# Kernel optimization log

Measured on AMD Instinct MI355X. Metric: run time of the kernel, lower is better.

The kernel has to match this reference:

```python
import jax, jax.numpy as jnp
import numpy as np

B, S, H, NH, PF, L, V = 8, 1024, 1024, 16, 4096, 6, 32000
HD = H // NH
STD = 0.02
NEG = -1e10


def setup_inputs() -> dict:
    key = jax.random.key(0)
    ks = jax.random.split(key, 12)
    inp = {
        "src": jax.random.randint(ks[0], (B, S), 0, V),
        "src_mask": jnp.ones((B, 1, 1, S), dtype=bool),
        "tok_emb": jax.random.normal(ks[1], (V, H), jnp.float32) * STD,
        "pos_emb": jax.random.normal(ks[2], (S, H), jnp.float32) * STD,
        "Wq": jax.random.normal(ks[3], (L, H, H), jnp.float32) * STD,
        "bq": jnp.zeros((L, H), jnp.float32),
        "Wk": jax.random.normal(ks[4], (L, H, H), jnp.float32) * STD,
        "bk": jnp.zeros((L, H), jnp.float32),
        "Wv": jax.random.normal(ks[5], (L, H, H), jnp.float32) * STD,
        "bv": jnp.zeros((L, H), jnp.float32),
        "Wo": jax.random.normal(ks[6], (L, H, H), jnp.float32) * STD,
        "bo": jnp.zeros((L, H), jnp.float32),
        "W1": jax.random.normal(ks[7], (L, H, PF), jnp.float32) * STD,
        "b1": jnp.zeros((L, PF), jnp.float32),
        "W2": jax.random.normal(ks[8], (L, PF, H), jnp.float32) * STD,
        "b2": jnp.zeros((L, H), jnp.float32),
        "ln1_g": jnp.ones((L, H), jnp.float32),
        "ln1_b": jnp.zeros((L, H), jnp.float32),
        "ln2_g": jnp.ones((L, H), jnp.float32),
        "ln2_b": jnp.zeros((L, H), jnp.float32),
    }
    return inp


def layer_norm(x, g, b, eps=1e-5):
    m = jnp.mean(x, axis=-1, keepdims=True)
    v = jnp.mean((x - m) ** 2, axis=-1, keepdims=True)
    return (x - m) * jax.lax.rsqrt(v + eps) * g + b


def reference(src, src_mask, tok_emb, pos_emb, Wq, bq, Wk, bk, Wv, bv, Wo, bo,
              W1, b1, W2, b2, ln1_g, ln1_b, ln2_g, ln2_b):
    # embedding * sqrt(hid_dim) + positional embedding (dropout = identity at eval)
    x = tok_emb[src] * jnp.sqrt(jnp.float32(H)) + pos_emb[None, :S]
    attn_scale = jnp.sqrt(jnp.float32(HD))
    for l in range(L):
        # multi-head self-attention
        q = (x @ Wq[l] + bq[l]).reshape(B, S, NH, HD).transpose(0, 2, 1, 3)
        k = (x @ Wk[l] + bk[l]).reshape(B, S, NH, HD).transpose(0, 2, 1, 3)
        v = (x @ Wv[l] + bv[l]).reshape(B, S, NH, HD).transpose(0, 2, 1, 3)
        energy = jnp.einsum('bhqd,bhkd->bhqk', q, k) / attn_scale  # [B,NH,S,S]
        energy = jnp.where(src_mask, energy, NEG)
        attn = jax.nn.softmax(energy, axis=-1)
        o = jnp.einsum('bhqk,bhkd->bhqd', attn, v)
        o = o.transpose(0, 2, 1, 3).reshape(B, S, H) @ Wo[l] + bo[l]
        x = layer_norm(x + o, ln1_g[l], ln1_b[l])
        # position-wise feedforward
        f = jax.nn.relu(x @ W1[l] + b1[l]) @ W2[l] + b2[l]
        x = layer_norm(x + f, ln2_g[l], ln2_b[l])
    return x
```

## Files before the change

### kernel.cpp

```cpp
#include <hip/hip_runtime.h>
#include <cstdint>
#include <cstddef>


#define DI __device__ __forceinline__

typedef __attribute__((ext_vector_type(8))) short short8;
typedef __attribute__((ext_vector_type(4))) short s16x4;
typedef __attribute__((ext_vector_type(4))) float f32x4;
typedef __attribute__((ext_vector_type(4))) unsigned u32x4;

static constexpr int H  = 1024;
static constexpr int S  = 1024;
static constexpr int BB = 8;
static constexpr int NH = 16;
static constexpr int PF = 4096;
static constexpr int M  = BB * S;
static constexpr int L  = 6;

DI short f2bf(float f) {
  unsigned u = __builtin_bit_cast(unsigned, f);
  u += 0x7fffu + ((u >> 16) & 1u);
  return (short)(u >> 16);
}

DI unsigned packbf(float a, float b) {
  return (__builtin_bit_cast(unsigned, a) >> 16) |
         (__builtin_bit_cast(unsigned, b) & 0xffff0000u);
}

DI void async16(void* lds, const void* g) {
  __builtin_amdgcn_global_load_lds(
      (const __attribute__((address_space(1))) unsigned*)g,
      (__attribute__((address_space(3))) unsigned*)lds, 16, 0, 0);
}

DI f32x4 mfma16(short8 a, short8 b, f32x4 c) {
  return __builtin_amdgcn_mfma_f32_16x16x32_bf16(a, b, c, 0, 0, 0);
}

__global__ __launch_bounds__(256) void embed_kernel(
    const int* __restrict__ src, const float* __restrict__ tok,
    const float* __restrict__ pos, float* __restrict__ xf,
    short* __restrict__ xb) {
  const int row = blockIdx.x;
  const int s = row & (S - 1);
  const int i0 = threadIdx.x << 2;
  const int v = src[row];
  const float4 te = *(const float4*)(tok + (size_t)v * H + i0);
  const float4 pe = *(const float4*)(pos + (size_t)s * H + i0);
  float o[4] = {te.x * 32.f + pe.x, te.y * 32.f + pe.y,
                te.z * 32.f + pe.z, te.w * 32.f + pe.w};
  *(float4*)(xf + (size_t)row * H + i0) = make_float4(o[0], o[1], o[2], o[3]);
  s16x4 pk;
  pk[0] = f2bf(o[0]); pk[1] = f2bf(o[1]); pk[2] = f2bf(o[2]); pk[3] = f2bf(o[3]);
  *(s16x4*)(xb + (size_t)row * H + i0) = pk;
}

__global__ __launch_bounds__(256) void wconv_kernel(
    const float* __restrict__ W, short* __restrict__ Wt, int K, int N) {
  __shared__ float tile[64][65];
  const int ntn = N >> 6;
  const int k0 = (blockIdx.x / ntn) << 6;
  const int n0 = (blockIdx.x % ntn) << 6;
  const int r4 = threadIdx.x >> 6, cc = threadIdx.x & 63;
#pragma unroll
  for (int i = 0; i < 16; i++) {
    const int r = (i << 2) + r4;
    tile[r][cc] = W[(size_t)(k0 + r) * N + n0 + cc];
  }
  __syncthreads();
#pragma unroll
  for (int i = 0; i < 16; i++) {
    const int n = (i << 2) + r4;
    Wt[(size_t)(n0 + n) * K + k0 + cc] = f2bf(tile[cc][n]);
  }
}

template <int EPI>
__global__ __launch_bounds__(256, 4) void gemm128(
    const short* __restrict__ A, const short* __restrict__ Bt,
    const float* __restrict__ bias, void* __restrict__ out,
    const int N, const int K) {
  __shared__ char lds[32768];
  const int tid = threadIdx.x;
  const int w = tid >> 6, lane = tid & 63;
  const int g = lane >> 4, ci = lane & 15;
  const int wm = w >> 1, wn = w & 1;
  const int nbn = N >> 7;
  const int bid = (int)blockIdx.x;
  const int swz = (bid & 7) * ((int)gridDim.x >> 3) + (bid >> 3);
  const int brow = (swz / nbn) << 7;
  const int bcol = (swz % nbn) << 7;

  const int srow = lane >> 2;
  const int schk = ((lane & 3) ^ ((lane >> 3) & 3)) << 3;
  const short* aS0 = A + (size_t)(brow + w * 16 + srow) * K + schk;
  const short* aS1 = A + (size_t)(brow + w * 16 + 64 + srow) * K + schk;
  const short* bS0 = Bt + (size_t)(bcol + w * 16 + srow) * K + schk;
  const short* bS1 = Bt + (size_t)(bcol + w * 16 + 64 + srow) * K + schk;

  int aoff[4], boff[4];
  const int swzc = (g ^ ((ci >> 1) & 3)) << 4;
#pragma unroll
  for (int i = 0; i < 4; i++) {
    aoff[i] = (wm * 64 + i * 16 + ci) * 64 + swzc;
    boff[i] = 8192 + (wn * 64 + i * 16 + ci) * 64 + swzc;
  }

  auto stage = [&](int kh, int buf) {
    char* base = lds + buf * 16384;
    const int ko = kh << 5;
    async16(base + w * 1024, aS0 + ko);
    async16(base + 4096 + w * 1024, aS1 + ko);
    async16(base + 8192 + w * 1024, bS0 + ko);
    async16(base + 12288 + w * 1024, bS1 + ko);
  };

  f32x4 acc[4][4];
#pragma unroll
  for (int a = 0; a < 4; a++)
#pragma unroll
    for (int c = 0; c < 4; c++) acc[a][c] = f32x4{0.f, 0.f, 0.f, 0.f};

  stage(0, 0);
  stage(1, 1);
  asm volatile("s_waitcnt vmcnt(4)" ::: "memory");
  __builtin_amdgcn_sched_barrier(0);
  __builtin_amdgcn_s_barrier();

  const int nt = K >> 5;
  for (int t = 0; t < nt; t++) {
    const char* cb = lds + (t & 1) * 16384;
    short8 afr[4], bfr[4];
#pragma unroll
    for (int mi = 0; mi < 4; mi++) afr[mi] = *(const short8*)(cb + aoff[mi]);
#pragma unroll
    for (int nj = 0; nj < 4; nj++) bfr[nj] = *(const short8*)(cb + boff[nj]);
    asm volatile("s_waitcnt lgkmcnt(0)" ::: "memory");
    __builtin_amdgcn_sched_barrier(0);
    __builtin_amdgcn_s_barrier();
    if (t + 2 < nt) stage(t + 2, t & 1);
    __builtin_amdgcn_s_setprio(1);
#pragma unroll
    for (int mi = 0; mi < 4; mi++)
#pragma unroll
      for (int nj = 0; nj < 4; nj++)
        acc[mi][nj] = mfma16(afr[mi], bfr[nj], acc[mi][nj]);
    __builtin_amdgcn_s_setprio(0);
    if (t + 2 < nt) asm volatile("s_waitcnt vmcnt(4)" ::: "memory");
    else            asm volatile("s_waitcnt vmcnt(0)" ::: "memory");
    __builtin_amdgcn_sched_barrier(0);
    if (t + 1 < nt) __builtin_amdgcn_s_barrier();
  }

  if constexpr (EPI <= 2) {
#pragma unroll
    for (int mi = 0; mi < 4; mi++) {
      float bv[4];
#pragma unroll
      for (int nj = 0; nj < 4; nj++)
        bv[nj] = bias[bcol + wn * 64 + nj * 16 + ci];
#pragma unroll
      for (int r = 0; r < 4; r++) {
        const int row = brow + wm * 64 + mi * 16 + (g << 2) + r;
#pragma unroll
        for (int nj = 0; nj < 4; nj++) {
          const int col = bcol + wn * 64 + nj * 16 + ci;
          float vv = acc[mi][nj][r] + bv[nj];
          if constexpr (EPI == 1) vv = fmaxf(vv, 0.f);
          if constexpr (EPI == 2) ((float*)out)[(size_t)row * N + col] = vv;
          else ((short*)out)[(size_t)row * N + col] = f2bf(vv);
        }
      }
    }
  } else {
    __syncthreads();
    short* bb = (short*)lds;
    const int bI = brow >> 10, s0 = brow & (S - 1);
    short* o = (short*)out;
#pragma unroll
    for (int hh = 0; hh < 2; hh++) {
      if (wn == hh) {
#pragma unroll
        for (int nj = 0; nj < 4; nj++) {
          const int d = nj * 16 + ci;
          const float bv = bias[bcol + hh * 64 + d];
#pragma unroll
          for (int mi = 0; mi < 4; mi++) {
            const int sl = wm * 64 + mi * 16 + (g << 2);
            s16x4 pk;
#pragma unroll
            for (int r = 0; r < 4; r++) pk[r] = f2bf(acc[mi][nj][r] + bv);
            *(s16x4*)(bb + d * 136 + sl) = pk;
          }
        }
      }
      __syncthreads();
#pragma unroll
      for (int jj = 0; jj < 4; jj++) {
        const int d = tid >> 2, sc = (tid & 3) + jj * 4;
        const short8 v = *(const short8*)(bb + d * 136 + sc * 8);
        *(short8*)(o + ((size_t)bI * H + bcol + hh * 64 + d) * S + s0 + sc * 8) = v;
      }
      __syncthreads();
    }
  }
}

__global__ __launch_bounds__(256) void attn_kernel(
    const short* __restrict__ q, const short* __restrict__ k,
    const short* __restrict__ vt, short* __restrict__ ao) {
  __shared__ short lsk[2][4096];
  __shared__ short lsv[2][4096];
  const int tid = threadIdx.x;
  const int w = tid >> 6, lane = tid & 63;
  const int g = lane >> 4, ci = lane & 15;
  const int bid = ((int)blockIdx.x & 7) * 256 + ((int)blockIdx.x >> 3);
  const int qt = bid & 15;
  const int bh = bid >> 4;
  const int b = bh >> 4, h = bh & 15;
  const int hbase = h << 6;

  const int r8 = lane >> 3, c8 = lane & 7;
  const int cs = c8 ^ r8;
  const short* kbase = k + ((size_t)b * S) * H + hbase;
  const short* vbase = vt + ((size_t)b * H + hbase) * S;

  const size_t qrow = (size_t)b * S + (qt << 6) + (w << 4) + ci;
  short8 qf[2];
#pragma unroll
  for (int ks = 0; ks < 2; ks++)
    qf[ks] = *(const short8*)(q + qrow * H + hbase + ks * 32 + (g << 3));

  const int swz = ci & 7;
  int koff[2], voff[2][2];
#pragma unroll
  for (int ks = 0; ks < 2; ks++) {
    koff[ks] = ci * 128 + (((4 * ks + g) ^ swz) << 4);
#pragma unroll
    for (int pc = 0; pc < 2; pc++)
      voff[ks][pc] =
          ci * 128 + (((4 * ks + 2 * pc + (g >> 1)) ^ swz) << 4) + ((g & 1) << 3);
  }

#pragma unroll
  for (int t = 0; t < 2; t++) {
    const int row = (w << 3) + t * 32 + r8;
    async16(&lsk[0][t * 2048 + (w << 9)], kbase + (size_t)row * H + cs * 8);
    async16(&lsv[0][t * 2048 + (w << 9)], vbase + (size_t)row * S + cs * 8);
  }
  __syncthreads();

  const f32x4 zero = {0.f, 0.f, 0.f, 0.f};
  f32x4 of[4];
#pragma unroll
  for (int nf = 0; nf < 4; nf++) of[nf] = zero;
  float mrun = -INFINITY, lsum = 0.f;

#pragma unroll 2
  for (int kt = 0; kt < 16; kt++) {
    const int cur = kt & 1;
    if (kt < 15) {
      const int kr1 = (kt + 1) << 6;
#pragma unroll
      for (int t = 0; t < 2; t++) {
        const int row = (w << 3) + t * 32 + r8;
        async16(&lsk[cur ^ 1][t * 2048 + (w << 9)],
                kbase + (size_t)(kr1 + row) * H + cs * 8);
        async16(&lsv[cur ^ 1][t * 2048 + (w << 9)],
                vbase + (size_t)row * S + kr1 + cs * 8);
      }
    }
    const char* kb = (const char*)lsk[cur];
    const char* vb = (const char*)lsv[cur];

    f32x4 st[4];
#pragma unroll
    for (int mf = 0; mf < 4; mf++) st[mf] = zero;
#pragma unroll
    for (int ks = 0; ks < 2; ks++)
#pragma unroll
      for (int mf = 0; mf < 4; mf++) {
        const short8 kf = *(const short8*)(kb + koff[ks] + mf * 2048);
        st[mf] = mfma16(kf, qf[ks], st[mf]);
      }

    float tmax = -INFINITY;
#pragma unroll
    for (int mf = 0; mf < 4; mf++)
#pragma unroll
      for (int r = 0; r < 4; r++) tmax = fmaxf(tmax, st[mf][r]);
    tmax = fmaxf(tmax, __shfl_xor(tmax, 16));
    tmax = fmaxf(tmax, __shfl_xor(tmax, 32));
    const float mnew = fmaxf(mrun, tmax * 0.125f);
    const float alpha = __expf(mrun - mnew);
    float rs = 0.f;
    float p[4][4];
#pragma unroll
    for (int mf = 0; mf < 4; mf++)
#pragma unroll
      for (int r = 0; r < 4; r++) {
        p[mf][r] = __expf(__builtin_fmaf(st[mf][r], 0.125f, -mnew));
        rs += p[mf][r];
      }
    rs += __shfl_xor(rs, 16);
    rs += __shfl_xor(rs, 32);
    lsum = lsum * alpha + rs;
    mrun = mnew;

    unsigned pk[4][2];
#pragma unroll
    for (int mf = 0; mf < 4; mf++) {
      pk[mf][0] = packbf(p[mf][0], p[mf][1]);
      pk[mf][1] = packbf(p[mf][2], p[mf][3]);
    }
#pragma unroll
    for (int nf = 0; nf < 4; nf++)
#pragma unroll
      for (int r = 0; r < 4; r++) of[nf][r] *= alpha;

#pragma unroll
    for (int ks = 0; ks < 2; ks++) {
      u32x4 uu;
      uu[0] = pk[2 * ks][0];
      uu[1] = pk[2 * ks][1];
      uu[2] = pk[2 * ks + 1][0];
      uu[3] = pk[2 * ks + 1][1];
      const short8 pfrag = __builtin_bit_cast(short8, uu);
#pragma unroll
      for (int nf = 0; nf < 4; nf++) {
        union { short8 v8; s16x4 h[2]; } vv;
        vv.h[0] = *(const s16x4*)(vb + voff[ks][0] + nf * 2048);
        vv.h[1] = *(const s16x4*)(vb + voff[ks][1] + nf * 2048);
        of[nf] = mfma16(vv.v8, pfrag, of[nf]);
      }
    }
    __syncthreads();
  }

  const float inv = 1.f / lsum;
#pragma unroll
  for (int nf = 0; nf < 4; nf++) {
    s16x4 o4;
#pragma unroll
    for (int r = 0; r < 4; r++) o4[r] = f2bf(of[nf][r] * inv);
    *(s16x4*)(ao + qrow * H + hbase + (nf << 4) + (g << 2)) = o4;
  }
}

__global__ __launch_bounds__(256) void ln_kernel(
    const float* __restrict__ x, const float* __restrict__ t,
    const float* __restrict__ gm, const float* __restrict__ bt,
    float* __restrict__ yf, short* __restrict__ yb) {
  const int row = blockIdx.x;
  const int i0 = threadIdx.x << 2;
  const size_t base = (size_t)row * H + i0;
  const float4 a = *(const float4*)(x + base);
  const float4 bb = *(const float4*)(t + base);
  float v[4] = {a.x + bb.x, a.y + bb.y, a.z + bb.z, a.w + bb.w};
  float s = v[0] + v[1] + v[2] + v[3];
  float qq = v[0] * v[0] + v[1] * v[1] + v[2] * v[2] + v[3] * v[3];
#pragma unroll
  for (int off = 32; off; off >>= 1) {
    s += __shfl_down(s, off);
    qq += __shfl_down(qq, off);
  }
  __shared__ float red[8];
  const int w = threadIdx.x >> 6, lane = threadIdx.x & 63;
  if (lane == 0) { red[w] = s; red[4 + w] = qq; }
  __syncthreads();
  s = red[0] + red[1] + red[2] + red[3];
  qq = red[4] + red[5] + red[6] + red[7];
  const float mean = s * (1.f / H);
  float var = qq * (1.f / H) - mean * mean;
  var = fmaxf(var, 0.f);
  const float rstd = rsqrtf(var + 1e-5f);
  const float4 gv = *(const float4*)(gm + i0);
  const float4 bv = *(const float4*)(bt + i0);
  float y[4] = {(v[0] - mean) * rstd * gv.x + bv.x,
                (v[1] - mean) * rstd * gv.y + bv.y,
                (v[2] - mean) * rstd * gv.z + bv.z,
                (v[3] - mean) * rstd * gv.w + bv.w};
  *(float4*)(yf + base) = make_float4(y[0], y[1], y[2], y[3]);
  s16x4 pk;
  pk[0] = f2bf(y[0]); pk[1] = f2bf(y[1]); pk[2] = f2bf(y[2]); pk[3] = f2bf(y[3]);
  *(s16x4*)(yb + base) = pk;
}

extern "C" void kernel_launch(void* const* d_in, const int* in_sizes, int n_in,
                              void* d_out, int out_size, void* d_ws, size_t ws_size,
                              hipStream_t stream) {
  const int* src = (const int*)d_in[0];
  const float* tok = (const float*)d_in[2];
  const float* pos = (const float*)d_in[3];
  const float* Wq = (const float*)d_in[4];
  const float* bq = (const float*)d_in[5];
  const float* Wk = (const float*)d_in[6];
  const float* bk = (const float*)d_in[7];
  const float* Wv = (const float*)d_in[8];
  const float* bv = (const float*)d_in[9];
  const float* Wo = (const float*)d_in[10];
  const float* bo = (const float*)d_in[11];
  const float* W1 = (const float*)d_in[12];
  const float* b1 = (const float*)d_in[13];
  const float* W2 = (const float*)d_in[14];
  const float* b2 = (const float*)d_in[15];
  const float* g1 = (const float*)d_in[16];
  const float* be1 = (const float*)d_in[17];
  const float* g2 = (const float*)d_in[18];
  const float* be2 = (const float*)d_in[19];

  char* p = (char*)d_ws;
  auto take = [&](size_t bytes) {
    char* r = p;
    p += (bytes + 255) & ~(size_t)255;
    return r;
  };
  float* xf   = (float*)take((size_t)M * H * 4);
  short* xb   = (short*)take((size_t)M * H * 2);
  float* tmp  = (float*)take((size_t)M * H * 4);
  short* qb   = (short*)take((size_t)M * H * 2);
  short* kbuf = (short*)take((size_t)M * H * 2);
  short* vtb  = (short*)take((size_t)M * H * 2);
  short* aob  = (short*)take((size_t)M * H * 2);
  short* fb   = (short*)take((size_t)M * PF * 2);
  short* wtq  = (short*)take((size_t)H * H * 2);
  short* wtk  = (short*)take((size_t)H * H * 2);
  short* wtv  = (short*)take((size_t)H * H * 2);
  short* wto  = (short*)take((size_t)H * H * 2);
  short* wt1  = (short*)take((size_t)H * PF * 2);
  short* wt2  = (short*)take((size_t)H * PF * 2);

  embed_kernel<<<M, 256, 0, stream>>>(src, tok, pos, xf, xb);

  for (int l = 0; l < L; l++) {
    wconv_kernel<<<(H / 64) * (H / 64), 256, 0, stream>>>(Wq + (size_t)l * H * H, wtq, H, H);
    wconv_kernel<<<(H / 64) * (H / 64), 256, 0, stream>>>(Wk + (size_t)l * H * H, wtk, H, H);
    wconv_kernel<<<(H / 64) * (H / 64), 256, 0, stream>>>(Wv + (size_t)l * H * H, wtv, H, H);
    wconv_kernel<<<(H / 64) * (H / 64), 256, 0, stream>>>(Wo + (size_t)l * H * H, wto, H, H);
    wconv_kernel<<<(H / 64) * (PF / 64), 256, 0, stream>>>(W1 + (size_t)l * H * PF, wt1, H, PF);
    wconv_kernel<<<(PF / 64) * (H / 64), 256, 0, stream>>>(W2 + (size_t)l * PF * H, wt2, PF, H);

    gemm128<0><<<512, 256, 0, stream>>>(xb, wtq, bq + (size_t)l * H, qb, H, H);
    gemm128<0><<<512, 256, 0, stream>>>(xb, wtk, bk + (size_t)l * H, kbuf, H, H);
    gemm128<3><<<512, 256, 0, stream>>>(xb, wtv, bv + (size_t)l * H, vtb, H, H);
    attn_kernel<<<BB * NH * (S / 64), 256, 0, stream>>>(qb, kbuf, vtb, aob);
    gemm128<2><<<512, 256, 0, stream>>>(aob, wto, bo + (size_t)l * H, tmp, H, H);
    ln_kernel<<<M, 256, 0, stream>>>(xf, tmp, g1 + (size_t)l * H, be1 + (size_t)l * H, xf, xb);
    gemm128<1><<<2048, 256, 0, stream>>>(xb, wt1, b1 + (size_t)l * PF, fb, PF, H);
    gemm128<2><<<512, 256, 0, stream>>>(fb, wt2, b2 + (size_t)l * H, tmp, H, PF);
    float* yf = (l == L - 1) ? (float*)d_out : xf;
    ln_kernel<<<M, 256, 0, stream>>>(xf, tmp, g2 + (size_t)l * H, be2 + (size_t)l * H, yf, xb);
  }
}
```

Baseline: 2.392 ms.

## Use 256x128 triple-buffered GEMM tiles, fuse QKV GEMM and weight conversions

```diff
diff --git a/kernel.cpp b/kernel.cpp
--- a/kernel.cpp
+++ b/kernel.cpp
@@ -57,12 +57,31 @@
   *(s16x4*)(xb + (size_t)row * H + i0) = pk;
 }
 
-__global__ __launch_bounds__(256) void wconv_kernel(
-    const float* __restrict__ W, short* __restrict__ Wt, int K, int N) {
+__global__ __launch_bounds__(256) void wconv_layer(
+    const float* __restrict__ Wq, const float* __restrict__ Wk,
+    const float* __restrict__ Wv, const float* __restrict__ Wo,
+    const float* __restrict__ W1, const float* __restrict__ W2,
+    const float* __restrict__ bq, const float* __restrict__ bk,
+    const float* __restrict__ bv, short* __restrict__ tq,
+    short* __restrict__ tk, short* __restrict__ tv, short* __restrict__ to,
+    short* __restrict__ t1, short* __restrict__ t2, float* __restrict__ bqkv) {
+  const int id = blockIdx.x;
+  if (id >= 3072) {
+    const int i = (id - 3072) * 256 + threadIdx.x;
+    bqkv[i] = (i < 1024) ? bq[i] : (i < 2048) ? bk[i - 1024] : bv[i - 2048];
+    return;
+  }
+  const float* W; short* Wt; int K, N, lb;
+  if (id < 256)       { W = Wq; Wt = tq; K = 1024; N = 1024; lb = id; }
+  else if (id < 512)  { W = Wk; Wt = tk; K = 1024; N = 1024; lb = id - 256; }
+  else if (id < 768)  { W = Wv; Wt = tv; K = 1024; N = 1024; lb = id - 512; }
+  else if (id < 1024) { W = Wo; Wt = to; K = 1024; N = 1024; lb = id - 768; }
+  else if (id < 2048) { W = W1; Wt = t1; K = 1024; N = 4096; lb = id - 1024; }
+  else                { W = W2; Wt = t2; K = 4096; N = 1024; lb = id - 2048; }
   __shared__ float tile[64][65];
   const int ntn = N >> 6;
-  const int k0 = (blockIdx.x / ntn) << 6;
-  const int n0 = (blockIdx.x % ntn) << 6;
+  const int k0 = (lb / ntn) << 6;
+  const int n0 = (lb % ntn) << 6;
   const int r4 = threadIdx.x >> 6, cc = threadIdx.x & 63;
 #pragma unroll
   for (int i = 0; i < 16; i++) {
@@ -78,69 +97,79 @@
 }
 
 template <int EPI>
-__global__ __launch_bounds__(256, 4) void gemm128(
+__global__ __launch_bounds__(512, 2) void gemmT(
     const short* __restrict__ A, const short* __restrict__ Bt,
-    const float* __restrict__ bias, void* __restrict__ out,
-    const int N, const int K) {
-  __shared__ char lds[32768];
+    const float* __restrict__ bias, void* __restrict__ out0,
+    short* __restrict__ outK, short* __restrict__ outV,
+    const int nbn, const int outN, const int K) {
+  extern __shared__ char lds[];
+  constexpr int BUF = 49152;
   const int tid = threadIdx.x;
   const int w = tid >> 6, lane = tid & 63;
   const int g = lane >> 4, ci = lane & 15;
   const int wm = w >> 1, wn = w & 1;
-  const int nbn = N >> 7;
+
   const int bid = (int)blockIdx.x;
-  const int swz = (bid & 7) * ((int)gridDim.x >> 3) + (bid >> 3);
-  const int brow = (swz / nbn) << 7;
-  const int bcol = (swz % nbn) << 7;
-
-  const int srow = lane >> 2;
-  const int schk = ((lane & 3) ^ ((lane >> 3) & 3)) << 3;
-  const short* aS0 = A + (size_t)(brow + w * 16 + srow) * K + schk;
-  const short* aS1 = A + (size_t)(brow + w * 16 + 64 + srow) * K + schk;
-  const short* bS0 = Bt + (size_t)(bcol + w * 16 + srow) * K + schk;
-  const short* bS1 = Bt + (size_t)(bcol + w * 16 + 64 + srow) * K + schk;
-
-  int aoff[4], boff[4];
-  const int swzc = (g ^ ((ci >> 1) & 3)) << 4;
-#pragma unroll
-  for (int i = 0; i < 4; i++) {
-    aoff[i] = (wm * 64 + i * 16 + ci) * 64 + swzc;
-    boff[i] = 8192 + (wn * 64 + i * 16 + ci) * 64 + swzc;
-  }
-
-  auto stage = [&](int kh, int buf) {
-    char* base = lds + buf * 16384;
-    const int ko = kh << 5;
-    async16(base + w * 1024, aS0 + ko);
-    async16(base + 4096 + w * 1024, aS1 + ko);
-    async16(base + 8192 + w * 1024, bS0 + ko);
-    async16(base + 12288 + w * 1024, bS1 + ko);
+  const int xcd = bid & 7, ii = bid >> 3;
+  const int bm = ((xcd & 3) << 3) | (ii & 7);
+  const int bn = (xcd >> 2) * (nbn >> 1) + (ii >> 3);
+  const int brow = bm << 8;
+  const int bcol = bn << 7;
+
+  const int srow = tid >> 3;
+  const int schk = ((tid & 7) ^ (srow & 7)) << 3;
+  const short* aS[4];
+#pragma unroll
+  for (int j = 0; j < 4; j++)
+    aS[j] = A + (size_t)(brow + srow + j * 64) * K + schk;
+  const short* bS[2];
+#pragma unroll
+  for (int j = 0; j < 2; j++)
+    bS[j] = Bt + (size_t)(bcol + srow + j * 64) * K + schk;
+
+  auto stA = [&](int t2, int j) {
+    async16(lds + (t2 % 3) * BUF + (tid + j * 512) * 16, aS[j] + (t2 << 6));
   };
+  auto stB = [&](int t2, int j) {
+    async16(lds + (t2 % 3) * BUF + 32768 + (tid + j * 512) * 16,
+            bS[j] + (t2 << 6));
+  };
+
+  int aoff[2], boff[2];
+#pragma unroll
+  for (int ks = 0; ks < 2; ks++) {
+    const int chk = ((ks * 4 + g) ^ (ci & 7)) << 4;
+    aoff[ks] = (wm * 64 + ci) * 128 + chk;
+    boff[ks] = 32768 + (wn * 64 + ci) * 128 + chk;
+  }
 
   f32x4 acc[4][4];
 #pragma unroll
   for (int a = 0; a < 4; a++)
 #pragma unroll
-    for (int c = 0; c < 4; c++) acc[a][c] = f32x4{0.f, 0.f, 0.f, 0.f};
-
-  stage(0, 0);
-  stage(1, 1);
-  asm volatile("s_waitcnt vmcnt(4)" ::: "memory");
+    for (int b = 0; b < 4; b++) acc[a][b] = f32x4{0.f, 0.f, 0.f, 0.f};
+
+  stA(0, 0); stA(0, 1); stB(0, 0); stA(0, 2); stA(0, 3); stB(0, 1);
+  stA(1, 0); stA(1, 1); stB(1, 0); stA(1, 2); stA(1, 3); stB(1, 1);
+  asm volatile("s_waitcnt vmcnt(6)" ::: "memory");
   __builtin_amdgcn_sched_barrier(0);
   __builtin_amdgcn_s_barrier();
 
-  const int nt = K >> 5;
+  const int nt = K >> 6;
   for (int t = 0; t < nt; t++) {
-    const char* cb = lds + (t & 1) * 16384;
+    const char* cb = lds + (t % 3) * BUF;
+    const bool pf = (t + 2 < nt);
     short8 afr[4], bfr[4];
 #pragma unroll
-    for (int mi = 0; mi < 4; mi++) afr[mi] = *(const short8*)(cb + aoff[mi]);
-#pragma unroll
-    for (int nj = 0; nj < 4; nj++) bfr[nj] = *(const short8*)(cb + boff[nj]);
+    for (int mi = 0; mi < 4; mi++)
+      afr[mi] = *(const short8*)(cb + aoff[0] + mi * 2048);
+#pragma unroll
+    for (int nj = 0; nj < 4; nj++)
+      bfr[nj] = *(const short8*)(cb + boff[0] + nj * 2048);
+    if (pf) { stA(t + 2, 0); stA(t + 2, 1); stB(t + 2, 0); }
+    __builtin_amdgcn_s_barrier();
     asm volatile("s_waitcnt lgkmcnt(0)" ::: "memory");
     __builtin_amdgcn_sched_barrier(0);
-    __builtin_amdgcn_s_barrier();
-    if (t + 2 < nt) stage(t + 2, t & 1);
     __builtin_amdgcn_s_setprio(1);
 #pragma unroll
     for (int mi = 0; mi < 4; mi++)
@@ -148,62 +177,86 @@
       for (int nj = 0; nj < 4; nj++)
         acc[mi][nj] = mfma16(afr[mi], bfr[nj], acc[mi][nj]);
     __builtin_amdgcn_s_setprio(0);
-    if (t + 2 < nt) asm volatile("s_waitcnt vmcnt(4)" ::: "memory");
-    else            asm volatile("s_waitcnt vmcnt(0)" ::: "memory");
+    __builtin_amdgcn_s_barrier();
+#pragma unroll
+    for (int mi = 0; mi < 4; mi++)
+      afr[mi] = *(const short8*)(cb + aoff[1] + mi * 2048);
+#pragma unroll
+    for (int nj = 0; nj < 4; nj++)
+      bfr[nj] = *(const short8*)(cb + boff[1] + nj * 2048);
+    if (pf) { stA(t + 2, 2); stA(t + 2, 3); stB(t + 2, 1); }
+    __builtin_amdgcn_s_barrier();
+    asm volatile("s_waitcnt lgkmcnt(0)" ::: "memory");
     __builtin_amdgcn_sched_barrier(0);
-    if (t + 1 < nt) __builtin_amdgcn_s_barrier();
-  }
-
-  if constexpr (EPI <= 2) {
+    __builtin_amdgcn_s_setprio(1);
+#pragma unroll
+    for (int mi = 0; mi < 4; mi++)
+#pragma unroll
+      for (int nj = 0; nj < 4; nj++)
+        acc[mi][nj] = mfma16(afr[mi], bfr[nj], acc[mi][nj]);
+    __builtin_amdgcn_s_setprio(0);
+    if (pf) asm volatile("s_waitcnt vmcnt(6)" ::: "memory");
+    else    asm volatile("s_waitcnt vmcnt(0)" ::: "memory");
+    __builtin_amdgcn_sched_barrier(0);
+    __builtin_amdgcn_s_barrier();
+  }
+
+  const bool vpath = (EPI == 4) && (bcol >= 2048);
+  if (!vpath) {
+    short* oq; const short* dummy; (void)dummy;
+    int bc = bcol;
+    if constexpr (EPI == 4) {
+      oq = (bcol >> 10) ? outK : (short*)out0;
+      bc = bcol & 1023;
+    }
+    float bv[4];
+#pragma unroll
+    for (int nj = 0; nj < 4; nj++)
+      bv[nj] = bias[bcol + wn * 64 + nj * 16 + ci];
 #pragma unroll
     for (int mi = 0; mi < 4; mi++) {
-      float bv[4];
-#pragma unroll
-      for (int nj = 0; nj < 4; nj++)
-        bv[nj] = bias[bcol + wn * 64 + nj * 16 + ci];
 #pragma unroll
       for (int r = 0; r < 4; r++) {
         const int row = brow + wm * 64 + mi * 16 + (g << 2) + r;
 #pragma unroll
         for (int nj = 0; nj < 4; nj++) {
-          const int col = bcol + wn * 64 + nj * 16 + ci;
+          const int col = bc + wn * 64 + nj * 16 + ci;
           float vv = acc[mi][nj][r] + bv[nj];
           if constexpr (EPI == 1) vv = fmaxf(vv, 0.f);
-          if constexpr (EPI == 2) ((float*)out)[(size_t)row * N + col] = vv;
-          else ((short*)out)[(size_t)row * N + col] = f2bf(vv);
-        }
-      }
-    }
-  } else {
-    __syncthreads();
-    short* bb = (short*)lds;
-    const int bI = brow >> 10, s0 = brow & (S - 1);
-    short* o = (short*)out;
-#pragma unroll
-    for (int hh = 0; hh < 2; hh++) {
-      if (wn == hh) {
-#pragma unroll
-        for (int nj = 0; nj < 4; nj++) {
-          const int d = nj * 16 + ci;
-          const float bv = bias[bcol + hh * 64 + d];
-#pragma unroll
-          for (int mi = 0; mi < 4; mi++) {
-            const int sl = wm * 64 + mi * 16 + (g << 2);
-            s16x4 pk;
-#pragma unroll
-            for (int r = 0; r < 4; r++) pk[r] = f2bf(acc[mi][nj][r] + bv);
-            *(s16x4*)(bb + d * 136 + sl) = pk;
+          if constexpr (EPI == 2) {
+            ((float*)out0)[(size_t)row * outN + col] = vv;
+          } else if constexpr (EPI == 4) {
+            oq[(size_t)row * outN + col] = f2bf(vv);
+          } else {
+            ((short*)out0)[(size_t)row * outN + col] = f2bf(vv);
           }
         }
       }
-      __syncthreads();
-#pragma unroll
-      for (int jj = 0; jj < 4; jj++) {
-        const int d = tid >> 2, sc = (tid & 3) + jj * 4;
-        const short8 v = *(const short8*)(bb + d * 136 + sc * 8);
-        *(short8*)(o + ((size_t)bI * H + bcol + hh * 64 + d) * S + s0 + sc * 8) = v;
+    }
+  } else {
+    __syncthreads();
+    short* tb = (short*)lds;
+#pragma unroll
+    for (int nj = 0; nj < 4; nj++) {
+      const int d = wn * 64 + nj * 16 + ci;
+      const float bv = bias[bcol + d];
+#pragma unroll
+      for (int mi = 0; mi < 4; mi++) {
+        const int s = wm * 64 + mi * 16 + (g << 2);
+        s16x4 pk;
+#pragma unroll
+        for (int r = 0; r < 4; r++) pk[r] = f2bf(acc[mi][nj][r] + bv);
+        *(s16x4*)(tb + d * 264 + s) = pk;
       }
-      __syncthreads();
+    }
+    __syncthreads();
+    const int b = brow >> 10, s0 = brow & (S - 1), d0 = bcol & 1023;
+#pragma unroll
+    for (int rr = 0; rr < 8; rr++) {
+      const int idx = tid + rr * 512;
+      const int d = idx >> 5, sc = idx & 31;
+      const short8 v = *(const short8*)(tb + d * 264 + sc * 8);
+      *(short8*)(outV + ((size_t)b * H + d0 + d) * S + s0 + sc * 8) = v;
     }
   }
 }
@@ -411,46 +464,56 @@
   const float* g2 = (const float*)d_in[18];
   const float* be2 = (const float*)d_in[19];
 
+  hipFuncSetAttribute(reinterpret_cast<const void*>(gemmT<1>),
+                      hipFuncAttributeMaxDynamicSharedMemorySize, 147456);
+  hipFuncSetAttribute(reinterpret_cast<const void*>(gemmT<2>),
+                      hipFuncAttributeMaxDynamicSharedMemorySize, 147456);
+  hipFuncSetAttribute(reinterpret_cast<const void*>(gemmT<4>),
+                      hipFuncAttributeMaxDynamicSharedMemorySize, 147456);
+
   char* p = (char*)d_ws;
   auto take = [&](size_t bytes) {
     char* r = p;
     p += (bytes + 255) & ~(size_t)255;
     return r;
   };
-  float* xf   = (float*)take((size_t)M * H * 4);
-  short* xb   = (short*)take((size_t)M * H * 2);
-  float* tmp  = (float*)take((size_t)M * H * 4);
-  short* qb   = (short*)take((size_t)M * H * 2);
-  short* kbuf = (short*)take((size_t)M * H * 2);
-  short* vtb  = (short*)take((size_t)M * H * 2);
-  short* aob  = (short*)take((size_t)M * H * 2);
-  short* fb   = (short*)take((size_t)M * PF * 2);
-  short* wtq  = (short*)take((size_t)H * H * 2);
-  short* wtk  = (short*)take((size_t)H * H * 2);
-  short* wtv  = (short*)take((size_t)H * H * 2);
-  short* wto  = (short*)take((size_t)H * H * 2);
-  short* wt1  = (short*)take((size_t)H * PF * 2);
-  short* wt2  = (short*)take((size_t)H * PF * 2);
+  float* xf    = (float*)take((size_t)M * H * 4);
+  short* xb    = (short*)take((size_t)M * H * 2);
+  float* tmp   = (float*)take((size_t)M * H * 4);
+  short* qb    = (short*)take((size_t)M * H * 2);
+  short* kbuf  = (short*)take((size_t)M * H * 2);
+  short* vtb   = (short*)take((size_t)M * H * 2);
+  short* aob   = (short*)take((size_t)M * H * 2);
+  short* fb    = (short*)take((size_t)M * PF * 2);
+  short* wtqkv = (short*)take((size_t)3 * H * H * 2);
+  short* wto   = (short*)take((size_t)H * H * 2);
+  short* wt1   = (short*)take((size_t)H * PF * 2);
+  short* wt2   = (short*)take((size_t)H * PF * 2);
+  float* bqkv  = (float*)take((size_t)3 * H * 4);
 
   embed_kernel<<<M, 256, 0, stream>>>(src, tok, pos, xf, xb);
 
   for (int l = 0; l < L; l++) {
-    wconv_kernel<<<(H / 64) * (H / 64), 256, 0, stream>>>(Wq + (size_t)l * H * H, wtq, H, H);
-    wconv_kernel<<<(H / 64) * (H / 64), 256, 0, stream>>>(Wk + (size_t)l * H * H, wtk, H, H);
-    wconv_kernel<<<(H / 64) * (H / 64), 256, 0, stream>>>(Wv + (size_t)l * H * H, wtv, H, H);
-    wconv_kernel<<<(H / 64) * (H / 64), 256, 0, stream>>>(Wo + (size_t)l * H * H, wto, H, H);
-    wconv_kernel<<<(H / 64) * (PF / 64), 256, 0, stream>>>(W1 + (size_t)l * H * PF, wt1, H, PF);
-    wconv_kernel<<<(PF / 64) * (H / 64), 256, 0, stream>>>(W2 + (size_t)l * PF * H, wt2, PF, H);
-
-    gemm128<0><<<512, 256, 0, stream>>>(xb, wtq, bq + (size_t)l * H, qb, H, H);
-    gemm128<0><<<512, 256, 0, stream>>>(xb, wtk, bk + (size_t)l * H, kbuf, H, H);
-    gemm128<3><<<512, 256, 0, stream>>>(xb, wtv, bv + (size_t)l * H, vtb, H, H);
+    wconv_layer<<<3084, 256, 0, stream>>>(
+        Wq + (size_t)l * H * H, Wk + (size_t)l * H * H, Wv + (size_t)l * H * H,
+        Wo + (size_t)l * H * H, W1 + (size_t)l * H * PF, W2 + (size_t)l * PF * H,
+        bq + (size_t)l * H, bk + (size_t)l * H, bv + (size_t)l * H,
+        wtqkv, wtqkv + (size_t)H * H, wtqkv + (size_t)2 * H * H,
+        wto, wt1, wt2, bqkv);
+
+    gemmT<4><<<768, 512, 147456, stream>>>(xb, wtqkv, bqkv, qb, kbuf, vtb,
+                                           24, H, H);
     attn_kernel<<<BB * NH * (S / 64), 256, 0, stream>>>(qb, kbuf, vtb, aob);
-    gemm128<2><<<512, 256, 0, stream>>>(aob, wto, bo + (size_t)l * H, tmp, H, H);
-    ln_kernel<<<M, 256, 0, stream>>>(xf, tmp, g1 + (size_t)l * H, be1 + (size_t)l * H, xf, xb);
-    gemm128<1><<<2048, 256, 0, stream>>>(xb, wt1, b1 + (size_t)l * PF, fb, PF, H);
-    gemm128<2><<<512, 256, 0, stream>>>(fb, wt2, b2 + (size_t)l * H, tmp, H, PF);
+    gemmT<2><<<256, 512, 147456, stream>>>(aob, wto, bo + (size_t)l * H, tmp,
+                                           nullptr, nullptr, 8, H, H);
+    ln_kernel<<<M, 256, 0, stream>>>(xf, tmp, g1 + (size_t)l * H,
+                                     be1 + (size_t)l * H, xf, xb);
+    gemmT<1><<<1024, 512, 147456, stream>>>(xb, wt1, b1 + (size_t)l * PF, fb,
+                                            nullptr, nullptr, 32, PF, H);
+    gemmT<2><<<256, 512, 147456, stream>>>(fb, wt2, b2 + (size_t)l * H, tmp,
+                                           nullptr, nullptr, 8, H, PF);
     float* yf = (l == L - 1) ? (float*)d_out : xf;
-    ln_kernel<<<M, 256, 0, stream>>>(xf, tmp, g2 + (size_t)l * H, be2 + (size_t)l * H, yf, xb);
-  }
-}
+    ln_kernel<<<M, 256, 0, stream>>>(xf, tmp, g2 + (size_t)l * H,
+                                     be2 + (size_t)l * H, yf, xb);
+  }
+}
```

Result: faster. 2.192 ms (-8.4%).
